# Optimization experiments

Hardware: AMD Instinct MI355X
Metric: run time of the kernel (lower is better)

The kernel has to match this reference:

```python
import jax, jax.numpy as jnp
import numpy as np

ALPHA = 0.7
BETA = 0.3


def setup_inputs() -> dict:
    key = jax.random.key(0)
    k1, k2 = jax.random.split(key)
    n = 8192
    predictions = jax.random.normal(k1, (n,), dtype=jnp.float32)
    # graded relevance labels in {0,1,2,3}, stored as float (torch code compares floats)
    targets = jax.random.randint(k2, (n,), 0, 4).astype(jnp.float32)
    return {"predictions": predictions, "targets": targets}


def reference(predictions, targets):
    # SmoothL1 (Huber, beta=1) with mean reduction
    d = predictions - targets
    ad = jnp.abs(d)
    huber = jnp.mean(jnp.where(ad < 1.0, 0.5 * d * d, ad - 0.5))

    # Pairwise hinge ranking loss over i<j pairs with targets[i] != targets[j].
    n = predictions.shape[0]
    pd = predictions[:, None] - predictions[None, :]   # [n, n] pred_i - pred_j
    td = targets[:, None] - targets[None, :]           # [n, n] targ_i - targ_j
    sign = jnp.where(td > 0, 1.0, -1.0)                # target_ranking
    idx = jnp.arange(n)
    mask = (td != 0) & (idx[:, None] < idx[None, :])   # upper triangle, unequal targets
    hinge = jnp.maximum(0.0, 1.0 - sign * pd)
    num = jnp.sum(jnp.where(mask, hinge, 0.0))
    cnt = jnp.sum(mask).astype(predictions.dtype)
    ranking = jnp.where(cnt > 0, num / jnp.maximum(cnt, 1.0), 0.0)

    return ALPHA * huber + BETA * ranking
```

## Files before the change

kernel.cpp:

```cpp
#include <hip/hip_runtime.h>

static constexpr int TILE = 128;


__global__ __launch_bounds__(TILE) void egl_pair_kernel(
    const float* __restrict__ pred, const float* __restrict__ targ, int n, int nT,
    float* __restrict__ ws_s, float* __restrict__ ws_c, float* __restrict__ ws_h) {
  int b = blockIdx.x;
  int ti = 0, rem = b;
  while (rem >= nT - ti) { rem -= (nT - ti); ++ti; }
  const int tj = ti + rem;

  __shared__ alignas(16) float2 sj[TILE];
  const int tid = threadIdx.x;
  const int j0 = tj * TILE;
  {
    int j = j0 + tid;
    float pj = (j < n) ? pred[j] : 0.0f;
    float tv = (j < n) ? targ[j] : 0.0f;
    sj[tid] = make_float2(pj, tv);
  }
  __syncthreads();

  const int i = ti * TILE + tid;
  const bool ivalid = (i < n);
  const float pi  = ivalid ? pred[i] : 0.0f;
  const float tiv = ivalid ? targ[i] : 0.0f;

  float s0 = 0.f, s1 = 0.f, s2 = 0.f, s3 = 0.f;
  float c0 = 0.f, c1 = 0.f, c2 = 0.f, c3 = 0.f;
  float hub = 0.f;

  const int jcount = min(TILE, n - j0);

  if (ti != tj) {
    if (ivalid) {
      if (jcount == TILE) {
        const float4* sj4 = (const float4*)sj;
#pragma unroll
        for (int k = 0; k < TILE / 2; k += 2) {
          float4 a = sj4[k];
          float4 bq = sj4[k + 1];
          { float sg = fminf(fmaxf(tiv - a.y, -1.f), 1.f);
            s0 += fmaxf(fmaf(-sg, pi - a.x, fabsf(sg)), 0.f); c0 += fabsf(sg); }
          { float sg = fminf(fmaxf(tiv - a.w, -1.f), 1.f);
            s1 += fmaxf(fmaf(-sg, pi - a.z, fabsf(sg)), 0.f); c1 += fabsf(sg); }
          { float sg = fminf(fmaxf(tiv - bq.y, -1.f), 1.f);
            s2 += fmaxf(fmaf(-sg, pi - bq.x, fabsf(sg)), 0.f); c2 += fabsf(sg); }
          { float sg = fminf(fmaxf(tiv - bq.w, -1.f), 1.f);
            s3 += fmaxf(fmaf(-sg, pi - bq.z, fabsf(sg)), 0.f); c3 += fabsf(sg); }
        }
      } else {
        for (int jj = 0; jj < jcount; ++jj) {
          float2 a = sj[jj];
          float sg = fminf(fmaxf(tiv - a.y, -1.f), 1.f);
          s0 += fmaxf(fmaf(-sg, pi - a.x, fabsf(sg)), 0.f);
          c0 += fabsf(sg);
        }
      }
    }
  } else {
    if (ivalid) {
      float d = pi - tiv;
      float ad = fabsf(d);
      hub = (ad < 1.0f) ? 0.5f * d * d : (ad - 0.5f);
      for (int jj = tid + 1; jj < jcount; ++jj) {
        float2 a = sj[jj];
        float sg = fminf(fmaxf(tiv - a.y, -1.f), 1.f);
        s0 += fmaxf(fmaf(-sg, pi - a.x, fabsf(sg)), 0.f);
        c0 += fabsf(sg);
      }
    }
  }

  float s = (s0 + s1) + (s2 + s3);
  float c = (c0 + c1) + (c2 + c3);

  for (int off = 32; off > 0; off >>= 1) {
    s   += __shfl_down(s, off, 64);
    c   += __shfl_down(c, off, 64);
    hub += __shfl_down(hub, off, 64);
  }
  __shared__ float red[2][3];
  if ((tid & 63) == 0) {
    int w = tid >> 6;
    red[w][0] = s; red[w][1] = c; red[w][2] = hub;
  }
  __syncthreads();
  if (tid == 0) {
    ws_s[b] = red[0][0] + red[1][0];
    ws_c[b] = red[0][1] + red[1][1];
    ws_h[b] = red[0][2] + red[1][2];
  }
}

__global__ __launch_bounds__(256) void egl_finalize(
    const float* __restrict__ ws_s, const float* __restrict__ ws_c,
    const float* __restrict__ ws_h, int nb, int n, float* __restrict__ out) {
  double s = 0.0, c = 0.0, h = 0.0;
  for (int idx = threadIdx.x; idx < nb; idx += 256) {
    s += (double)ws_s[idx];
    c += (double)ws_c[idx];
    h += (double)ws_h[idx];
  }
  for (int off = 32; off > 0; off >>= 1) {
    s += __shfl_down(s, off, 64);
    c += __shfl_down(c, off, 64);
    h += __shfl_down(h, off, 64);
  }
  __shared__ double red[4][3];
  int w = threadIdx.x >> 6;
  if ((threadIdx.x & 63) == 0) { red[w][0] = s; red[w][1] = c; red[w][2] = h; }
  __syncthreads();
  if (threadIdx.x == 0) {
    double S = 0.0, C = 0.0, H = 0.0;
    for (int k = 0; k < 4; ++k) { S += red[k][0]; C += red[k][1]; H += red[k][2]; }
    double huber = H / (double)n;
    double rank = (C > 0.0) ? (S / fmax(C, 1.0)) : 0.0;
    out[0] = (float)(0.7 * huber + 0.3 * rank);
  }
}

extern "C" void kernel_launch(void* const* d_in, const int* in_sizes, int n_in,
                              void* d_out, int out_size, void* d_ws, size_t ws_size,
                              hipStream_t stream) {
  const float* pred = (const float*)d_in[0];
  const float* targ = (const float*)d_in[1];
  const int n = in_sizes[0];

  const int nT = (n + TILE - 1) / TILE;
  const int nb = nT * (nT + 1) / 2;

  float* ws_s = (float*)d_ws;
  float* ws_c = ws_s + nb;
  float* ws_h = ws_c + nb;

  egl_pair_kernel<<<nb, TILE, 0, stream>>>(pred, targ, n, nT, ws_s, ws_c, ws_h);
  egl_finalize<<<1, 256, 0, stream>>>(ws_s, ws_c, ws_h, nb, n, (float*)d_out);
}
```

Measured before the change: 69.94 us.

## Fuse finalize into pair kernel via last-block atomic and split j-range across 256 threads

Each block now runs 256 threads: two halves of 128 threads share the same i-row and each processes half of the j tile. This doubles the number of waves per block and halves the per-thread inner loop. The separate finalize kernel is removed. A threadfence plus an atomic counter lets the last block perform the final double-precision reduction, and a memset on the workspace counter is added before launch. The aim is less launch overhead and better latency hiding, in exchange for an extra memset and atomic traffic.

```diff
diff --git a/kernel.cpp b/kernel.cpp
--- a/kernel.cpp
+++ b/kernel.cpp
@@ -1,20 +1,27 @@
 #include <hip/hip_runtime.h>
 
-static constexpr int TILE = 128;
+static constexpr int TI = 128;
+static constexpr int NTHREADS = 256;
 
 
-__global__ __launch_bounds__(TILE) void egl_pair_kernel(
+__global__ __launch_bounds__(NTHREADS) void egl_fused_kernel(
     const float* __restrict__ pred, const float* __restrict__ targ, int n, int nT,
-    float* __restrict__ ws_s, float* __restrict__ ws_c, float* __restrict__ ws_h) {
-  int b = blockIdx.x;
-  int ti = 0, rem = b;
+    unsigned int* __restrict__ counter,
+    float* __restrict__ ws_s, float* __restrict__ ws_c, float* __restrict__ ws_h,
+    float* __restrict__ out) {
+  const int nb = gridDim.x;
+
+  int bidx = blockIdx.x;
+  int ti = 0, rem = bidx;
   while (rem >= nT - ti) { rem -= (nT - ti); ++ti; }
   const int tj = ti + rem;
 
-  __shared__ alignas(16) float2 sj[TILE];
-  const int tid = threadIdx.x;
-  const int j0 = tj * TILE;
-  {
+  __shared__ alignas(16) float2 sj[TI];
+  const int tid  = threadIdx.x;
+  const int il   = tid & (TI - 1);
+  const int half = tid >> 7;
+  const int j0 = tj * TI;
+  if (tid < TI) {
     int j = j0 + tid;
     float pj = (j < n) ? pred[j] : 0.0f;
     float tv = (j < n) ? targ[j] : 0.0f;
@@ -22,7 +29,7 @@
   }
   __syncthreads();
 
-  const int i = ti * TILE + tid;
+  const int i = ti * TI + il;
   const bool ivalid = (i < n);
   const float pi  = ivalid ? pred[i] : 0.0f;
   const float tiv = ivalid ? targ[i] : 0.0f;
@@ -31,40 +38,45 @@
   float c0 = 0.f, c1 = 0.f, c2 = 0.f, c3 = 0.f;
   float hub = 0.f;
 
-  const int jcount = min(TILE, n - j0);
+  const int jcount = min(TI, n - j0);
 
   if (ti != tj) {
-    if (ivalid) {
-      if (jcount == TILE) {
-        const float4* sj4 = (const float4*)sj;
+    if (ivalid && jcount == TI) {
+      const float4* sj4 = (const float4*)sj;
+      const int k0 = half * 32;
 #pragma unroll
-        for (int k = 0; k < TILE / 2; k += 2) {
-          float4 a = sj4[k];
-          float4 bq = sj4[k + 1];
-          { float sg = fminf(fmaxf(tiv - a.y, -1.f), 1.f);
-            s0 += fmaxf(fmaf(-sg, pi - a.x, fabsf(sg)), 0.f); c0 += fabsf(sg); }
-          { float sg = fminf(fmaxf(tiv - a.w, -1.f), 1.f);
-            s1 += fmaxf(fmaf(-sg, pi - a.z, fabsf(sg)), 0.f); c1 += fabsf(sg); }
-          { float sg = fminf(fmaxf(tiv - bq.y, -1.f), 1.f);
-            s2 += fmaxf(fmaf(-sg, pi - bq.x, fabsf(sg)), 0.f); c2 += fabsf(sg); }
-          { float sg = fminf(fmaxf(tiv - bq.w, -1.f), 1.f);
-            s3 += fmaxf(fmaf(-sg, pi - bq.z, fabsf(sg)), 0.f); c3 += fabsf(sg); }
-        }
-      } else {
-        for (int jj = 0; jj < jcount; ++jj) {
-          float2 a = sj[jj];
-          float sg = fminf(fmaxf(tiv - a.y, -1.f), 1.f);
-          s0 += fmaxf(fmaf(-sg, pi - a.x, fabsf(sg)), 0.f);
-          c0 += fabsf(sg);
-        }
+      for (int k = k0; k < k0 + 32; k += 2) {
+        float4 a = sj4[k];
+        float4 bq = sj4[k + 1];
+        { float sg = fminf(fmaxf(tiv - a.y, -1.f), 1.f);
+          s0 += fmaxf(fmaf(-sg, pi - a.x, fabsf(sg)), 0.f); c0 += fabsf(sg); }
+        { float sg = fminf(fmaxf(tiv - a.w, -1.f), 1.f);
+          s1 += fmaxf(fmaf(-sg, pi - a.z, fabsf(sg)), 0.f); c1 += fabsf(sg); }
+        { float sg = fminf(fmaxf(tiv - bq.y, -1.f), 1.f);
+          s2 += fmaxf(fmaf(-sg, pi - bq.x, fabsf(sg)), 0.f); c2 += fabsf(sg); }
+        { float sg = fminf(fmaxf(tiv - bq.w, -1.f), 1.f);
+          s3 += fmaxf(fmaf(-sg, pi - bq.z, fabsf(sg)), 0.f); c3 += fabsf(sg); }
+      }
+    } else if (ivalid) {
+      const int jlo = half * 64;
+      const int jhi = min(jlo + 64, jcount);
+      for (int jj = jlo; jj < jhi; ++jj) {
+        float2 a = sj[jj];
+        float sg = fminf(fmaxf(tiv - a.y, -1.f), 1.f);
+        s0 += fmaxf(fmaf(-sg, pi - a.x, fabsf(sg)), 0.f);
+        c0 += fabsf(sg);
       }
     }
   } else {
     if (ivalid) {
-      float d = pi - tiv;
-      float ad = fabsf(d);
-      hub = (ad < 1.0f) ? 0.5f * d * d : (ad - 0.5f);
-      for (int jj = tid + 1; jj < jcount; ++jj) {
+      if (half == 0) {
+        float d = pi - tiv;
+        float ad = fabsf(d);
+        hub = (ad < 1.0f) ? 0.5f * d * d : (ad - 0.5f);
+      }
+      const int jlo = max(il + 1, half * 64);
+      const int jhi = min(half * 64 + 64, jcount);
+      for (int jj = jlo; jj < jhi; ++jj) {
         float2 a = sj[jj];
         float sg = fminf(fmaxf(tiv - a.y, -1.f), 1.f);
         s0 += fmaxf(fmaf(-sg, pi - a.x, fabsf(sg)), 0.f);
@@ -81,40 +93,45 @@
     c   += __shfl_down(c, off, 64);
     hub += __shfl_down(hub, off, 64);
   }
-  __shared__ float red[2][3];
+  __shared__ float red[4][3];
+  __shared__ bool is_last;
   if ((tid & 63) == 0) {
     int w = tid >> 6;
     red[w][0] = s; red[w][1] = c; red[w][2] = hub;
   }
   __syncthreads();
   if (tid == 0) {
-    ws_s[b] = red[0][0] + red[1][0];
-    ws_c[b] = red[0][1] + red[1][1];
-    ws_h[b] = red[0][2] + red[1][2];
+    ws_s[bidx] = (red[0][0] + red[1][0]) + (red[2][0] + red[3][0]);
+    ws_c[bidx] = (red[0][1] + red[1][1]) + (red[2][1] + red[3][1]);
+    ws_h[bidx] = (red[0][2] + red[1][2]) + (red[2][2] + red[3][2]);
+    __threadfence();
+    unsigned int v = atomicAdd(counter, 1u);
+    is_last = (v == (unsigned int)(nb - 1));
   }
-}
+  __syncthreads();
+  if (!is_last) return;
 
-__global__ __launch_bounds__(256) void egl_finalize(
-    const float* __restrict__ ws_s, const float* __restrict__ ws_c,
-    const float* __restrict__ ws_h, int nb, int n, float* __restrict__ out) {
-  double s = 0.0, c = 0.0, h = 0.0;
-  for (int idx = threadIdx.x; idx < nb; idx += 256) {
-    s += (double)ws_s[idx];
-    c += (double)ws_c[idx];
-    h += (double)ws_h[idx];
+  __threadfence();
+  double ds = 0.0, dc = 0.0, dh = 0.0;
+  for (int idx = tid; idx < nb; idx += NTHREADS) {
+    ds += (double)ws_s[idx];
+    dc += (double)ws_c[idx];
+    dh += (double)ws_h[idx];
   }
   for (int off = 32; off > 0; off >>= 1) {
-    s += __shfl_down(s, off, 64);
-    c += __shfl_down(c, off, 64);
-    h += __shfl_down(h, off, 64);
+    ds += __shfl_down(ds, off, 64);
+    dc += __shfl_down(dc, off, 64);
+    dh += __shfl_down(dh, off, 64);
   }
-  __shared__ double red[4][3];
-  int w = threadIdx.x >> 6;
-  if ((threadIdx.x & 63) == 0) { red[w][0] = s; red[w][1] = c; red[w][2] = h; }
+  __shared__ double dred[4][3];
+  if ((tid & 63) == 0) {
+    int w = tid >> 6;
+    dred[w][0] = ds; dred[w][1] = dc; dred[w][2] = dh;
+  }
   __syncthreads();
-  if (threadIdx.x == 0) {
+  if (tid == 0) {
     double S = 0.0, C = 0.0, H = 0.0;
-    for (int k = 0; k < 4; ++k) { S += red[k][0]; C += red[k][1]; H += red[k][2]; }
+    for (int k = 0; k < 4; ++k) { S += dred[k][0]; C += dred[k][1]; H += dred[k][2]; }
     double huber = H / (double)n;
     double rank = (C > 0.0) ? (S / fmax(C, 1.0)) : 0.0;
     out[0] = (float)(0.7 * huber + 0.3 * rank);
@@ -128,13 +145,15 @@
   const float* targ = (const float*)d_in[1];
   const int n = in_sizes[0];
 
-  const int nT = (n + TILE - 1) / TILE;
+  const int nT = (n + TI - 1) / TI;
   const int nb = nT * (nT + 1) / 2;
 
-  float* ws_s = (float*)d_ws;
+  unsigned int* counter = (unsigned int*)d_ws;
+  float* ws_s = (float*)((char*)d_ws + 16);
   float* ws_c = ws_s + nb;
   float* ws_h = ws_c + nb;
 
-  egl_pair_kernel<<<nb, TILE, 0, stream>>>(pred, targ, n, nT, ws_s, ws_c, ws_h);
-  egl_finalize<<<1, 256, 0, stream>>>(ws_s, ws_c, ws_h, nb, n, (float*)d_out);
+  hipMemsetAsync(d_ws, 0, 4, stream);
+  egl_fused_kernel<<<nb, NTHREADS, 0, stream>>>(pred, targ, n, nT, counter,
+                                                ws_s, ws_c, ws_h, (float*)d_out);
 }
```

Measured after the change: 103.2 us. 47.5% more time.

## Split each tile's j-range across two thread halves and vectorize diagonal tiles

Applied to the files above, without the earlier changes.

Blocks go from 128 to 256 threads. Each i row is now handled by two threads, each taking half of the 128 j columns, so the per-thread serial loop is halved and each block runs more waves. Diagonal tiles now use the unrolled float4 path, with a predicate that zeroes pairs where j <= i, in place of a divergent scalar loop. The cost is the same number of blocks, each with more threads, and a 4-wave reduction at the end.

```diff
diff --git a/kernel.cpp b/kernel.cpp
--- a/kernel.cpp
+++ b/kernel.cpp
@@ -1,20 +1,57 @@
 #include <hip/hip_runtime.h>
 
-static constexpr int TILE = 128;
+static constexpr int TI = 128;
+static constexpr int NTHREADS = 256;
 
 
-__global__ __launch_bounds__(TILE) void egl_pair_kernel(
+template <bool DIAG>
+__device__ __forceinline__ void accum_tile(const float4* __restrict__ sj4,
+                                           float pi, float tiv, int il, int half,
+                                           float& s0, float& s1, float& s2, float& s3,
+                                           float& c0, float& c1, float& c2, float& c3) {
+  const int k0 = half * 32;
+#pragma unroll
+  for (int k = 0; k < 32; k += 2) {
+    float4 a = sj4[k0 + k];
+    float4 b = sj4[k0 + k + 1];
+    const int jb = 2 * (k0 + k);
+    {
+      float sg = fminf(fmaxf(tiv - a.y, -1.f), 1.f);
+      if (DIAG) sg = (jb + 0 > il) ? sg : 0.f;
+      s0 += fmaxf(fmaf(-sg, pi - a.x, fabsf(sg)), 0.f); c0 += fabsf(sg);
+    }
+    {
+      float sg = fminf(fmaxf(tiv - a.w, -1.f), 1.f);
+      if (DIAG) sg = (jb + 1 > il) ? sg : 0.f;
+      s1 += fmaxf(fmaf(-sg, pi - a.z, fabsf(sg)), 0.f); c1 += fabsf(sg);
+    }
+    {
+      float sg = fminf(fmaxf(tiv - b.y, -1.f), 1.f);
+      if (DIAG) sg = (jb + 2 > il) ? sg : 0.f;
+      s2 += fmaxf(fmaf(-sg, pi - b.x, fabsf(sg)), 0.f); c2 += fabsf(sg);
+    }
+    {
+      float sg = fminf(fmaxf(tiv - b.w, -1.f), 1.f);
+      if (DIAG) sg = (jb + 3 > il) ? sg : 0.f;
+      s3 += fmaxf(fmaf(-sg, pi - b.z, fabsf(sg)), 0.f); c3 += fabsf(sg);
+    }
+  }
+}
+
+__global__ __launch_bounds__(NTHREADS) void egl_pair_kernel(
     const float* __restrict__ pred, const float* __restrict__ targ, int n, int nT,
     float* __restrict__ ws_s, float* __restrict__ ws_c, float* __restrict__ ws_h) {
-  int b = blockIdx.x;
-  int ti = 0, rem = b;
+  int bidx = blockIdx.x;
+  int ti = 0, rem = bidx;
   while (rem >= nT - ti) { rem -= (nT - ti); ++ti; }
   const int tj = ti + rem;
 
-  __shared__ alignas(16) float2 sj[TILE];
-  const int tid = threadIdx.x;
-  const int j0 = tj * TILE;
-  {
+  __shared__ alignas(16) float2 sj[TI];
+  const int tid  = threadIdx.x;
+  const int il   = tid & (TI - 1);
+  const int half = tid >> 7;
+  const int j0 = tj * TI;
+  if (tid < TI) {
     int j = j0 + tid;
     float pj = (j < n) ? pred[j] : 0.0f;
     float tv = (j < n) ? targ[j] : 0.0f;
@@ -22,7 +59,7 @@
   }
   __syncthreads();
 
-  const int i = ti * TILE + tid;
+  const int i = ti * TI + il;
   const bool ivalid = (i < n);
   const float pi  = ivalid ? pred[i] : 0.0f;
   const float tiv = ivalid ? targ[i] : 0.0f;
@@ -31,44 +68,40 @@
   float c0 = 0.f, c1 = 0.f, c2 = 0.f, c3 = 0.f;
   float hub = 0.f;
 
-  const int jcount = min(TILE, n - j0);
+  const int jcount = min(TI, n - j0);
+  const float4* sj4 = (const float4*)sj;
 
-  if (ti != tj) {
-    if (ivalid) {
-      if (jcount == TILE) {
-        const float4* sj4 = (const float4*)sj;
-#pragma unroll
-        for (int k = 0; k < TILE / 2; k += 2) {
-          float4 a = sj4[k];
-          float4 bq = sj4[k + 1];
-          { float sg = fminf(fmaxf(tiv - a.y, -1.f), 1.f);
-            s0 += fmaxf(fmaf(-sg, pi - a.x, fabsf(sg)), 0.f); c0 += fabsf(sg); }
-          { float sg = fminf(fmaxf(tiv - a.w, -1.f), 1.f);
-            s1 += fmaxf(fmaf(-sg, pi - a.z, fabsf(sg)), 0.f); c1 += fabsf(sg); }
-          { float sg = fminf(fmaxf(tiv - bq.y, -1.f), 1.f);
-            s2 += fmaxf(fmaf(-sg, pi - bq.x, fabsf(sg)), 0.f); c2 += fabsf(sg); }
-          { float sg = fminf(fmaxf(tiv - bq.w, -1.f), 1.f);
-            s3 += fmaxf(fmaf(-sg, pi - bq.z, fabsf(sg)), 0.f); c3 += fabsf(sg); }
-        }
+  if (ivalid) {
+    if (ti != tj) {
+      if (jcount == TI) {
+        accum_tile<false>(sj4, pi, tiv, il, half, s0, s1, s2, s3, c0, c1, c2, c3);
       } else {
-        for (int jj = 0; jj < jcount; ++jj) {
+        const int jlo = half * 64;
+        const int jhi = min(jlo + 64, jcount);
+        for (int jj = jlo; jj < jhi; ++jj) {
           float2 a = sj[jj];
           float sg = fminf(fmaxf(tiv - a.y, -1.f), 1.f);
           s0 += fmaxf(fmaf(-sg, pi - a.x, fabsf(sg)), 0.f);
           c0 += fabsf(sg);
         }
       }
-    }
-  } else {
-    if (ivalid) {
-      float d = pi - tiv;
-      float ad = fabsf(d);
-      hub = (ad < 1.0f) ? 0.5f * d * d : (ad - 0.5f);
-      for (int jj = tid + 1; jj < jcount; ++jj) {
-        float2 a = sj[jj];
-        float sg = fminf(fmaxf(tiv - a.y, -1.f), 1.f);
-        s0 += fmaxf(fmaf(-sg, pi - a.x, fabsf(sg)), 0.f);
-        c0 += fabsf(sg);
+    } else {
+      if (half == 0) {
+        float d = pi - tiv;
+        float ad = fabsf(d);
+        hub = (ad < 1.0f) ? 0.5f * d * d : (ad - 0.5f);
+      }
+      if (jcount == TI) {
+        accum_tile<true>(sj4, pi, tiv, il, half, s0, s1, s2, s3, c0, c1, c2, c3);
+      } else {
+        const int jlo = max(il + 1, half * 64);
+        const int jhi = min(half * 64 + 64, jcount);
+        for (int jj = jlo; jj < jhi; ++jj) {
+          float2 a = sj[jj];
+          float sg = fminf(fmaxf(tiv - a.y, -1.f), 1.f);
+          s0 += fmaxf(fmaf(-sg, pi - a.x, fabsf(sg)), 0.f);
+          c0 += fabsf(sg);
+        }
       }
     }
   }
@@ -81,16 +114,16 @@
     c   += __shfl_down(c, off, 64);
     hub += __shfl_down(hub, off, 64);
   }
-  __shared__ float red[2][3];
+  __shared__ float red[4][3];
   if ((tid & 63) == 0) {
     int w = tid >> 6;
     red[w][0] = s; red[w][1] = c; red[w][2] = hub;
   }
   __syncthreads();
   if (tid == 0) {
-    ws_s[b] = red[0][0] + red[1][0];
-    ws_c[b] = red[0][1] + red[1][1];
-    ws_h[b] = red[0][2] + red[1][2];
+    ws_s[bidx] = (red[0][0] + red[1][0]) + (red[2][0] + red[3][0]);
+    ws_c[bidx] = (red[0][1] + red[1][1]) + (red[2][1] + red[3][1]);
+    ws_h[bidx] = (red[0][2] + red[1][2]) + (red[2][2] + red[3][2]);
   }
 }
 
@@ -128,13 +161,13 @@
   const float* targ = (const float*)d_in[1];
   const int n = in_sizes[0];
 
-  const int nT = (n + TILE - 1) / TILE;
+  const int nT = (n + TI - 1) / TI;
   const int nb = nT * (nT + 1) / 2;
 
   float* ws_s = (float*)d_ws;
   float* ws_c = ws_s + nb;
   float* ws_h = ws_c + nb;
 
-  egl_pair_kernel<<<nb, TILE, 0, stream>>>(pred, targ, n, nT, ws_s, ws_c, ws_h);
+  egl_pair_kernel<<<nb, NTHREADS, 0, stream>>>(pred, targ, n, nT, ws_s, ws_c, ws_h);
   egl_finalize<<<1, 256, 0, stream>>>(ws_s, ws_c, ws_h, nb, n, (float*)d_out);
 }
```

Result: faster. 67.03 us (-4.2%).
